# Optimization experiments

Measured on AMD Instinct MI355X. Metric: run time of the kernel, lower is better.

The kernel has to match this reference:

```python
import jax, jax.numpy as jnp
import numpy as np
from jax import lax

B, N, C = 8, 2000, 81            # batch, proposals, classes
MAX_INST = 100                    # config.detection_max_instances
MIN_CONF = 0.05                   # config.detection_min_confidence
NMS_THR = 0.3                     # config.detection_nms_threshold
H, W = 512, 512                   # config.image_shape[:2]
CLASS_OFFSET = 2.0                # > window extent, separates classes for batched NMS


def setup_inputs() -> dict:
    key = jax.random.key(0)
    k1, k2, k3, k4 = jax.random.split(key, 4)
    # valid normalized boxes (y1<y2, x1<x2)
    ctr = jax.random.uniform(k1, (B, N, 2))
    sz = jax.random.uniform(k2, (B, N, 2), minval=0.02, maxval=0.25)
    lo = jnp.clip(ctr - sz / 2, 0.0, 1.0)
    hi = jnp.clip(ctr + sz / 2, 0.0, 1.0)
    rois = jnp.stack([lo[..., 0], lo[..., 1], hi[..., 0], hi[..., 1]], axis=-1)
    probs = jax.nn.softmax(4.0 * jax.random.normal(k3, (B, N, C)), axis=-1)
    deltas = 0.1 * jax.random.normal(k4, (B, N, C, 4))
    bbox_std_dev = jnp.array([0.1, 0.1, 0.2, 0.2], jnp.float32)
    return {"rois": rois, "probs": probs, "deltas": deltas,
            "bbox_std_dev": bbox_std_dev}


def _apply_box_deltas(boxes, d):
    # boxes [N,4] (y1,x1,y2,x2), d [N,4] (dy,dx,log dh,log dw)
    h = boxes[:, 2] - boxes[:, 0]
    w = boxes[:, 3] - boxes[:, 1]
    cy = boxes[:, 0] + 0.5 * h + d[:, 0] * h
    cx = boxes[:, 1] + 0.5 * w + d[:, 1] * w
    h = h * jnp.exp(d[:, 2])
    w = w * jnp.exp(d[:, 3])
    return jnp.stack([cy - 0.5 * h, cx - 0.5 * w, cy + 0.5 * h, cx + 0.5 * w], axis=1)


def _pairwise_iou(b):
    # b [N,4] -> [N,N]
    area = (b[:, 2] - b[:, 0]) * (b[:, 3] - b[:, 1])
    yy1 = jnp.maximum(b[:, None, 0], b[None, :, 0])
    xx1 = jnp.maximum(b[:, None, 1], b[None, :, 1])
    yy2 = jnp.minimum(b[:, None, 2], b[None, :, 2])
    xx2 = jnp.minimum(b[:, None, 3], b[None, :, 3])
    inter = jnp.maximum(yy2 - yy1, 0.0) * jnp.maximum(xx2 - xx1, 0.0)
    union = area[:, None] + area[None, :] - inter
    return inter / jnp.maximum(union, 1e-12)


def _refine_one(rois, probs, deltas, bbox_std_dev):
    # rois [N,4], probs [N,C], deltas [N,C,4]
    cls = jnp.argmax(probs, axis=1)                       # [N] int
    idx = jnp.arange(N)
    scores = probs[idx, cls]                              # [N]
    d = deltas[idx, cls] * bbox_std_dev                   # [N,4]
    refined = jnp.clip(_apply_box_deltas(rois, d), 0.0, 1.0)  # window (0,0,1,1)
    valid = (cls > 0) & (scores >= MIN_CONF)
    # sort by score desc; invalid last
    order = jnp.argsort(-jnp.where(valid, scores, -jnp.inf))
    b = refined[order]
    s = scores[order]
    c = cls[order]
    v = valid[order]
    # per-class NMS via class-offset trick (equivalent to per-class NMS)
    ob = b + CLASS_OFFSET * c[:, None].astype(b.dtype)
    iou = _pairwise_iou(ob)                               # [N,N]

    def body(i, carry):
        keep, counts = carry
        sup = jnp.any(keep & (iou[i] > NMS_THR))
        ci = c[i]
        ok = v[i] & (~sup) & (counts[ci] < MAX_INST)      # per-class max_output_size
        return keep.at[i].set(ok), counts.at[ci].add(ok.astype(jnp.int32))

    keep, _ = lax.fori_loop(0, N, body,
                            (jnp.zeros((N,), bool), jnp.zeros((C,), jnp.int32)))
    kscores = jnp.where(keep, s, -jnp.inf)
    topv, topi = lax.top_k(kscores, MAX_INST)             # global top-k, sorted
    dvalid = topv > -jnp.inf
    boxes = jnp.where(dvalid[:, None], b[topi], 0.0)
    cls_f = jnp.where(dvalid, c[topi].astype(jnp.float32), 0.0)
    scr = jnp.where(dvalid, topv, 0.0)
    return jnp.concatenate([boxes, cls_f[:, None], scr[:, None]], axis=1)  # [MAX_INST,6]


def _attention_mask(det):
    # det [B,MAX_INST,6]; padded rows are all-zero boxes -> cover no pixels
    ys = (jnp.arange(H, dtype=jnp.float32) + 0.5) / H
    xs = (jnp.arange(W, dtype=jnp.float32) + 0.5) / W
    iny = (ys >= det[:, :, 0:1]) & (ys < det[:, :, 2:3])  # [B,D,H]
    inx = (xs >= det[:, :, 1:2]) & (xs < det[:, :, 3:4])  # [B,D,W]
    m = jnp.einsum('bdh,bdw->bhw', iny.astype(jnp.float32), inx.astype(jnp.float32))
    return (m > 0).astype(jnp.float32)


def reference(rois, probs, deltas, bbox_std_dev):
    det = jax.vmap(lambda r, p, dl: _refine_one(r, p, dl, bbox_std_dev))(rois, probs, deltas)
    mask = _attention_mask(det)
    return det, mask
```

## Files before the change

kernel.cpp:

```cpp
#include <hip/hip_runtime.h>
#include <math.h>

#define BB 8
#define NN 2000
#define CC 81
#define NPAD 2048
#define MAXI 100
#define HH 512
#define WW 512

__global__ void k_refine(const float* __restrict__ rois,
                         const float* __restrict__ probs,
                         const float* __restrict__ deltas,
                         const float* __restrict__ stdv,
                         float* __restrict__ score, int* __restrict__ cls,
                         int* __restrict__ valid, float* __restrict__ box,
                         unsigned long long* __restrict__ gkeys) {
#pragma clang fp contract(off)
  int g = blockIdx.x * 4 + (threadIdx.x >> 6);
  if (g >= BB * NPAD) return;
  int lane = threadIdx.x & 63;
  int b = g >> 11, n = g & (NPAD - 1);
  if (n >= NN) {
    if (lane == 0) {
      unsigned u = __float_as_uint(-INFINITY);
      u = ~u;
      gkeys[b * NPAD + n] =
          ((unsigned long long)u << 32) | (0xFFFFFFFFu - (unsigned)n);
      valid[b * NPAD + n] = 0;
    }
    return;
  }
  const float* pp = probs + ((size_t)b * NN + n) * CC;
  float best = -INFINITY;
  int bc = CC;
  for (int c = lane; c < CC; c += 64) {
    float p = pp[c];
    if (p > best) { best = p; bc = c; }
  }
  for (int off = 32; off; off >>= 1) {
    float ob = __shfl_xor(best, off, 64);
    int oc = __shfl_xor(bc, off, 64);
    if (ob > best || (ob == best && oc < bc)) { best = ob; bc = oc; }
  }
  if (lane == 0) {
    int idx = b * NPAD + n;
    const float* r = rois + ((size_t)b * NN + n) * 4;
    const float* dd = deltas + (((size_t)b * NN + n) * CC + bc) * 4;
    float d0 = dd[0] * stdv[0], d1 = dd[1] * stdv[1];
    float d2 = dd[2] * stdv[2], d3 = dd[3] * stdv[3];
    float y1 = r[0], x1 = r[1], y2 = r[2], x2 = r[3];
    float h = y2 - y1, w = x2 - x1;
    float cy = y1 + 0.5f * h + d0 * h;
    float cx = x1 + 0.5f * w + d1 * w;
    h = h * (float)exp((double)d2);
    w = w * (float)exp((double)d3);
    float ny1 = cy - 0.5f * h, nx1 = cx - 0.5f * w;
    float ny2 = cy + 0.5f * h, nx2 = cx + 0.5f * w;
    ny1 = fminf(fmaxf(ny1, 0.f), 1.f);
    nx1 = fminf(fmaxf(nx1, 0.f), 1.f);
    ny2 = fminf(fmaxf(ny2, 0.f), 1.f);
    nx2 = fminf(fmaxf(nx2, 0.f), 1.f);
    box[idx * 4 + 0] = ny1;
    box[idx * 4 + 1] = nx1;
    box[idx * 4 + 2] = ny2;
    box[idx * 4 + 3] = nx2;
    score[idx] = best;
    cls[idx] = bc;
    int v = (bc > 0 && best >= 0.05f) ? 1 : 0;
    valid[idx] = v;
    float ks = v ? best : -INFINITY;
    unsigned u = __float_as_uint(ks);
    u = (u & 0x80000000u) ? ~u : (u | 0x80000000u);
    gkeys[idx] = ((unsigned long long)u << 32) | (0xFFFFFFFFu - (unsigned)n);
  }
}

__global__ void k_rankp(const unsigned long long* __restrict__ gkeys,
                        int* __restrict__ partial) {
  __shared__ unsigned long long sk[256];
  int blk = blockIdx.x;
  int jp = blk & 7, ip = (blk >> 3) & 7, b = blk >> 6;
  int tid = threadIdx.x;
  sk[tid] = gkeys[b * NPAD + jp * 256 + tid];
  unsigned long long myk = gkeys[b * NPAD + ip * 256 + tid];
  __syncthreads();
  int cnt = 0;
#pragma unroll 8
  for (int j = 0; j < 256; j++) cnt += (sk[j] > myk) ? 1 : 0;
  partial[(b * 8 + jp) * NPAD + ip * 256 + tid] = cnt;
}

__global__ void __launch_bounds__(256)
k_permnms(const int* __restrict__ partial, const float* __restrict__ score,
          const int* __restrict__ cls, const int* __restrict__ valid,
          const float* __restrict__ box, float* __restrict__ det) {
#pragma clang fp contract(off)
  __shared__ int sperm[NPAD];
  int b = blockIdx.x, tid = threadIdx.x;
  for (int e = tid; e < NPAD; e += 256) {
    int rank = 0;
#pragma unroll
    for (int jp = 0; jp < 8; jp++) rank += partial[(b * 8 + jp) * NPAD + e];
    sperm[rank] = e;
  }
  __syncthreads();
  if (tid >= 64) return;
  int lane = tid;
  int kept = 0;
  bool done = false;
  float k0y1 = 0.f, k0x1 = 0.f, k0y2 = 0.f, k0x2 = 0.f, k0a = 0.f;
  float k1y1 = 0.f, k1x1 = 0.f, k1y2 = 0.f, k1x2 = 0.f, k1a = 0.f;
  for (int base = 0; base < NN && !done; base += 64) {
    int pi = sperm[base + lane];
    int o = b * NPAD + pi;
    float4 bx = ((const float4*)box)[o];
    int lv = valid[o];
    int lc = cls[o];
    float lsc = score[o];
    int lim = (NN - base < 64) ? (NN - base) : 64;
    for (int j = 0; j < lim; j++) {
      int v = __shfl(lv, j, 64);
      if (!v) { done = true; break; }
      float y1 = __shfl(bx.x, j, 64);
      float x1 = __shfl(bx.y, j, 64);
      float y2 = __shfl(bx.z, j, 64);
      float x2 = __shfl(bx.w, j, 64);
      int c = __shfl(lc, j, 64);
      float off = 2.0f * (float)c;
      float oy1 = y1 + off, ox1 = x1 + off, oy2 = y2 + off, ox2 = x2 + off;
      float area_i = (oy2 - oy1) * (ox2 - ox1);
      bool pred = false;
      if (lane < kept) {
        float yy1 = fmaxf(oy1, k0y1), xx1 = fmaxf(ox1, k0x1);
        float yy2 = fminf(oy2, k0y2), xx2 = fminf(ox2, k0x2);
        float inter = fmaxf(yy2 - yy1, 0.f) * fmaxf(xx2 - xx1, 0.f);
        float uni = (area_i + k0a) - inter;
        pred = (inter / fmaxf(uni, 1e-12f)) > 0.3f;
      }
      if (64 + lane < kept) {
        float yy1 = fmaxf(oy1, k1y1), xx1 = fmaxf(ox1, k1x1);
        float yy2 = fminf(oy2, k1y2), xx2 = fminf(ox2, k1x2);
        float inter = fmaxf(yy2 - yy1, 0.f) * fmaxf(xx2 - xx1, 0.f);
        float uni = (area_i + k1a) - inter;
        pred = pred || ((inter / fmaxf(uni, 1e-12f)) > 0.3f);
      }
      if (__ballot(pred) == 0ULL) {
        if (kept < 64) {
          if (lane == kept) { k0y1 = oy1; k0x1 = ox1; k0y2 = oy2; k0x2 = ox2; k0a = area_i; }
        } else {
          if (lane == kept - 64) { k1y1 = oy1; k1x1 = ox1; k1y2 = oy2; k1x2 = ox2; k1a = area_i; }
        }
        float sc = __shfl(lsc, j, 64);
        if (lane == 0) {
          float* dr = det + ((size_t)b * MAXI + kept) * 6;
          dr[0] = y1; dr[1] = x1; dr[2] = y2; dr[3] = x2;
          dr[4] = (float)c; dr[5] = sc;
        }
        kept++;
        if (kept == MAXI) { done = true; break; }
      }
    }
  }
  int rem = (MAXI - kept) * 6;
  float* dr0 = det + ((size_t)b * MAXI + kept) * 6;
  for (int t = lane; t < rem; t += 64) dr0[t] = 0.f;
}

__global__ void k_mask(const float* __restrict__ det, float* __restrict__ mask) {
  __shared__ float lx1[MAXI], lx2[MAXI];
  __shared__ unsigned long long wmask[4];
  int x = blockIdx.x;
  int h = x & (HH - 1);
  int b = x >> 9;
  int tid = threadIdx.x;
  int wv = tid >> 6, ln = tid & 63;
  float ys = ((float)h + 0.5f) * (1.0f / 512.0f);
  bool inb = false;
  float bx1 = 0.f, bx2 = 0.f;
  if (tid < MAXI) {
    const float* dr = det + ((size_t)b * MAXI + tid) * 6;
    float y1 = dr[0], y2 = dr[2];
    bx1 = dr[1]; bx2 = dr[3];
    inb = (ys >= y1 && ys < y2);
  }
  unsigned long long bm = __ballot(inb);
  if (ln == 0) wmask[wv] = bm;
  __syncthreads();
  int n = __popcll(wmask[0]) + __popcll(wmask[1]);
  if (inb) {
    int pos = (wv ? __popcll(wmask[0]) : 0) +
              __popcll(bm & ((1ULL << ln) - 1ULL));
    lx1[pos] = bx1; lx2[pos] = bx2;
  }
  __syncthreads();
  float xs0 = ((float)tid + 0.5f) * (1.0f / 512.0f);
  float xs1 = ((float)(tid + 256) + 0.5f) * (1.0f / 512.0f);
  bool c0 = false, c1 = false;
  for (int t = 0; t < n; t++) {
    float a = lx1[t], bq = lx2[t];
    c0 = c0 || (xs0 >= a && xs0 < bq);
    c1 = c1 || (xs1 >= a && xs1 < bq);
  }
  float* row = mask + ((size_t)b * HH + h) * WW;
  row[tid] = c0 ? 1.0f : 0.0f;
  row[tid + 256] = c1 ? 1.0f : 0.0f;
}

extern "C" void kernel_launch(void* const* d_in, const int* in_sizes, int n_in,
                              void* d_out, int out_size, void* d_ws, size_t ws_size,
                              hipStream_t stream) {
  const float* rois = (const float*)d_in[0];
  const float* probs = (const float*)d_in[1];
  const float* deltas = (const float*)d_in[2];
  const float* stdv = (const float*)d_in[3];
  float* out = (float*)d_out;
  float* det = out;
  float* mask = out + BB * MAXI * 6;

  char* p = (char*)d_ws;
  unsigned long long* gkeys = (unsigned long long*)p; p += (size_t)BB * NPAD * 8;
  float* box     = (float*)p; p += (size_t)BB * NPAD * 16;
  float* score   = (float*)p; p += (size_t)BB * NPAD * 4;
  int*   cls     = (int*)p;   p += (size_t)BB * NPAD * 4;
  int*   valid   = (int*)p;   p += (size_t)BB * NPAD * 4;
  int*   partial = (int*)p;   p += (size_t)BB * 8 * NPAD * 4;

  k_refine<<<(BB * NPAD) / 4, 256, 0, stream>>>(rois, probs, deltas, stdv,
                                                score, cls, valid, box, gkeys);
  k_rankp<<<BB * 64, 256, 0, stream>>>(gkeys, partial);
  k_permnms<<<BB, 256, 0, stream>>>(partial, score, cls, valid, box, det);
  k_mask<<<BB * HH, 256, 0, stream>>>(det, mask);
}
```

Before: 136.3 us.

## Parallelize NMS with block-wide IoU bitmask tiles and a wave-level greedy scan

The single-wave sequential greedy NMS is replaced by a 256-wide tile scheme. All 256 threads first compute suppression against the already-kept boxes, then build a 256x256 pairwise IoU bitmask in shared memory. One wave then resolves the greedy keep order with ballots and bit operations, and writes the kept detections. This is meant to cut the long serial shuffle chain per candidate. In exchange it does a full 256x256 IoU tile of work per chunk and adds block-wide barriers.

```diff
diff --git a/kernel.cpp b/kernel.cpp
--- a/kernel.cpp
+++ b/kernel.cpp
@@ -97,74 +97,146 @@
           const float* __restrict__ box, float* __restrict__ det) {
 #pragma clang fp contract(off)
   __shared__ int sperm[NPAD];
+  __shared__ float4 spk4[256];
+  __shared__ float sarea[256];
+  __shared__ float4 sbox4[256];
+  __shared__ float sscr[256];
+  __shared__ int   scl[256];
+  __shared__ int   sval[256];
+  __shared__ int   sksup[256];
+  __shared__ unsigned long long smask[256][5];
+  __shared__ float4 kpk4[MAXI];
+  __shared__ float  karea[MAXI];
+  __shared__ int s_kcount, s_done;
+
   int b = blockIdx.x, tid = threadIdx.x;
+  int lane = tid & 63, wv = tid >> 6;
+
   for (int e = tid; e < NPAD; e += 256) {
     int rank = 0;
 #pragma unroll
     for (int jp = 0; jp < 8; jp++) rank += partial[(b * 8 + jp) * NPAD + e];
     sperm[rank] = e;
   }
+  if (tid == 0) { s_kcount = 0; s_done = 0; }
   __syncthreads();
-  if (tid >= 64) return;
-  int lane = tid;
-  int kept = 0;
-  bool done = false;
-  float k0y1 = 0.f, k0x1 = 0.f, k0y2 = 0.f, k0x2 = 0.f, k0a = 0.f;
-  float k1y1 = 0.f, k1x1 = 0.f, k1y2 = 0.f, k1x2 = 0.f, k1a = 0.f;
-  for (int base = 0; base < NN && !done; base += 64) {
-    int pi = sperm[base + lane];
-    int o = b * NPAD + pi;
-    float4 bx = ((const float4*)box)[o];
-    int lv = valid[o];
-    int lc = cls[o];
-    float lsc = score[o];
-    int lim = (NN - base < 64) ? (NN - base) : 64;
-    for (int j = 0; j < lim; j++) {
-      int v = __shfl(lv, j, 64);
-      if (!v) { done = true; break; }
-      float y1 = __shfl(bx.x, j, 64);
-      float x1 = __shfl(bx.y, j, 64);
-      float y2 = __shfl(bx.z, j, 64);
-      float x2 = __shfl(bx.w, j, 64);
-      int c = __shfl(lc, j, 64);
+
+  int prevkept = 0;
+  for (int base = 0;; base += 256) {
+    {
+      int i = base + tid;
+      float4 bx = make_float4(0.f, 0.f, 0.f, 0.f);
+      int c = 0, v = 0;
+      float sc = 0.f;
+      if (i < NN) {
+        int o = b * NPAD + sperm[i];
+        bx = ((const float4*)box)[o];
+        c = cls[o]; v = valid[o]; sc = score[o];
+      }
       float off = 2.0f * (float)c;
-      float oy1 = y1 + off, ox1 = x1 + off, oy2 = y2 + off, ox2 = x2 + off;
-      float area_i = (oy2 - oy1) * (ox2 - ox1);
-      bool pred = false;
-      if (lane < kept) {
-        float yy1 = fmaxf(oy1, k0y1), xx1 = fmaxf(ox1, k0x1);
-        float yy2 = fminf(oy2, k0y2), xx2 = fminf(ox2, k0x2);
+      float oy1 = bx.x + off, ox1 = bx.y + off;
+      float oy2 = bx.z + off, ox2 = bx.w + off;
+      float ar = (oy2 - oy1) * (ox2 - ox1);
+      if (!v) { oy1 = ox1 = oy2 = ox2 = 0.f; ar = 0.f; }
+      spk4[tid] = make_float4(oy1, ox1, oy2, ox2);
+      sarea[tid] = ar;
+      sbox4[tid] = bx;
+      sscr[tid] = sc; scl[tid] = c; sval[tid] = v;
+    }
+    __syncthreads();
+    {
+      float4 me = spk4[tid];
+      float ma = sarea[tid];
+      int ks = 0;
+      int kc = s_kcount;
+      for (int t = 0; t < kc; t++) {
+        float4 kb = kpk4[t];
+        float yy1 = fmaxf(me.x, kb.x), xx1 = fmaxf(me.y, kb.y);
+        float yy2 = fminf(me.z, kb.z), xx2 = fminf(me.w, kb.w);
         float inter = fmaxf(yy2 - yy1, 0.f) * fmaxf(xx2 - xx1, 0.f);
-        float uni = (area_i + k0a) - inter;
-        pred = (inter / fmaxf(uni, 1e-12f)) > 0.3f;
-      }
-      if (64 + lane < kept) {
-        float yy1 = fmaxf(oy1, k1y1), xx1 = fmaxf(ox1, k1x1);
-        float yy2 = fminf(oy2, k1y2), xx2 = fminf(ox2, k1x2);
+        float uni = (ma + karea[t]) - inter;
+        if (inter / fmaxf(uni, 1e-12f) > 0.3f) ks = 1;
+      }
+      sksup[tid] = ks;
+      unsigned long long m0 = 0, m1 = 0, m2 = 0, m3 = 0;
+      for (int j = 0; j < 256; j++) {
+        float4 ob = spk4[j];
+        float yy1 = fmaxf(me.x, ob.x), xx1 = fmaxf(me.y, ob.y);
+        float yy2 = fminf(me.z, ob.z), xx2 = fminf(me.w, ob.w);
         float inter = fmaxf(yy2 - yy1, 0.f) * fmaxf(xx2 - xx1, 0.f);
-        float uni = (area_i + k1a) - inter;
-        pred = pred || ((inter / fmaxf(uni, 1e-12f)) > 0.3f);
-      }
-      if (__ballot(pred) == 0ULL) {
-        if (kept < 64) {
-          if (lane == kept) { k0y1 = oy1; k0x1 = ox1; k0y2 = oy2; k0x2 = ox2; k0a = area_i; }
-        } else {
-          if (lane == kept - 64) { k1y1 = oy1; k1x1 = ox1; k1y2 = oy2; k1x2 = ox2; k1a = area_i; }
+        float uni = (ma + sarea[j]) - inter;
+        unsigned long long bit =
+            (inter / fmaxf(uni, 1e-12f) > 0.3f) ? 1ULL : 0ULL;
+        if (j < 64) m0 |= bit << j;
+        else if (j < 128) m1 |= bit << (j - 64);
+        else if (j < 192) m2 |= bit << (j - 128);
+        else m3 |= bit << (j - 192);
+      }
+      smask[tid][0] = m0; smask[tid][1] = m1;
+      smask[tid][2] = m2; smask[tid][3] = m3;
+    }
+    __syncthreads();
+    if (wv == 0) {
+      unsigned long long m[4][4];
+      int rv[4], ok4[4];
+      for (int s = 0; s < 4; s++) {
+        int i = s * 64 + lane;
+        m[s][0] = smask[i][0]; m[s][1] = smask[i][1];
+        m[s][2] = smask[i][2]; m[s][3] = smask[i][3];
+        rv[s] = sval[i];
+        ok4[s] = rv[s] && !sksup[i];
+      }
+      unsigned long long vb0 = __ballot(rv[0] != 0);
+      unsigned long long vb1 = __ballot(rv[1] != 0);
+      unsigned long long vb2 = __ballot(rv[2] != 0);
+      unsigned long long vb3 = __ballot(rv[3] != 0);
+      bool all_valid = (vb0 & vb1 & vb2 & vb3) == ~0ULL;
+      unsigned long long acc[4] = {0ULL, 0ULL, 0ULL, 0ULL};
+      int kcount = prevkept;
+      bool stop = false;
+      for (int s = 0; s < 4 && !stop; s++) {
+        bool ok = ok4[s] && (((m[s][0] & acc[0]) | (m[s][1] & acc[1]) |
+                              (m[s][2] & acc[2]) | (m[s][3] & acc[3])) == 0ULL);
+        unsigned long long bal = __ballot(ok);
+        while (bal) {
+          int o = __ffsll((unsigned long long)bal) - 1;
+          acc[s] |= 1ULL << o;
+          kcount++;
+          if (kcount == MAXI) { stop = true; break; }
+          bool conf = ((m[s][s] >> o) & 1ULL) != 0ULL;
+          ok = ok && !conf && (lane != o);
+          bal = __ballot(ok);
         }
-        float sc = __shfl(lsc, j, 64);
-        if (lane == 0) {
-          float* dr = det + ((size_t)b * MAXI + kept) * 6;
-          dr[0] = y1; dr[1] = x1; dr[2] = y2; dr[3] = x2;
-          dr[4] = (float)c; dr[5] = sc;
+      }
+      int prefix[4], run = 0;
+      for (int s = 0; s < 4; s++) { prefix[s] = run; run += (int)__popcll(acc[s]); }
+      for (int s = 0; s < 4; s++) {
+        if ((acc[s] >> lane) & 1ULL) {
+          int i = s * 64 + lane;
+          int row = prevkept + prefix[s] +
+                    (int)__popcll(acc[s] & ((1ULL << lane) - 1ULL));
+          float4 bx = sbox4[i];
+          float* dr = det + ((size_t)b * MAXI + row) * 6;
+          dr[0] = bx.x; dr[1] = bx.y; dr[2] = bx.z; dr[3] = bx.w;
+          dr[4] = (float)scl[i]; dr[5] = sscr[i];
+          kpk4[row] = spk4[i];
+          karea[row] = sarea[i];
         }
-        kept++;
-        if (kept == MAXI) { done = true; break; }
+      }
+      if (lane == 0) {
+        s_kcount = kcount;
+        s_done = (kcount >= MAXI) || !all_valid || (base + 256 >= NN) ? 1 : 0;
       }
     }
-  }
-  int rem = (MAXI - kept) * 6;
-  float* dr0 = det + ((size_t)b * MAXI + kept) * 6;
-  for (int t = lane; t < rem; t += 64) dr0[t] = 0.f;
+    __syncthreads();
+    prevkept = s_kcount;
+    if (s_done) break;
+  }
+  {
+    int rem = (MAXI - prevkept) * 6;
+    float* dr0 = det + ((size_t)b * MAXI + prevkept) * 6;
+    for (int t = tid; t < rem; t += 256) dr0[t] = 0.f;
+  }
 }
 
 __global__ void k_mask(const float* __restrict__ det, float* __restrict__ mask) {
```

New measurement: 163.3 us. 1.2x slower.

## Precompute IoU bitmask for top-256 candidates and resolve NMS via ballots

Applied to the files above, without the earlier changes.

Grows the NMS block to 1024 threads. The block builds a 256x256 pairwise suppression bitmask in shared memory for the top-ranked candidates, then one wave resolves greedy NMS with bitmask ANDs and ballot loops instead of one serial IoU pass per candidate. The old serial shuffle loop is kept as a fallback for candidates past 256, and only runs when fewer than MAXI boxes are kept and all 256 were valid. This targets the long serial dependency chain in single-wave NMS, in exchange for more shared memory and an extra O(256^2) IoU computation.

```diff
diff --git a/kernel.cpp b/kernel.cpp
--- a/kernel.cpp
+++ b/kernel.cpp
@@ -91,80 +91,193 @@
   partial[(b * 8 + jp) * NPAD + ip * 256 + tid] = cnt;
 }
 
-__global__ void __launch_bounds__(256)
+__global__ void __launch_bounds__(1024)
 k_permnms(const int* __restrict__ partial, const float* __restrict__ score,
           const int* __restrict__ cls, const int* __restrict__ valid,
           const float* __restrict__ box, float* __restrict__ det) {
 #pragma clang fp contract(off)
   __shared__ int sperm[NPAD];
+  __shared__ float4 spk4[256];
+  __shared__ float sarea[256];
+  __shared__ float4 sbox4[256];
+  __shared__ float sscr[256];
+  __shared__ int   scl[256];
+  __shared__ int   sval[256];
+  __shared__ unsigned long long smask[256][5];
+  __shared__ float4 kpk4[MAXI];
+  __shared__ float  karea[MAXI];
+  __shared__ int s_kcount, s_need;
+
   int b = blockIdx.x, tid = threadIdx.x;
-  for (int e = tid; e < NPAD; e += 256) {
+  int lane = tid & 63, wv = tid >> 6;
+
+  for (int e = tid; e < NPAD; e += 1024) {
     int rank = 0;
 #pragma unroll
     for (int jp = 0; jp < 8; jp++) rank += partial[(b * 8 + jp) * NPAD + e];
     sperm[rank] = e;
   }
-  __syncthreads();
-  if (tid >= 64) return;
-  int lane = tid;
-  int kept = 0;
-  bool done = false;
-  float k0y1 = 0.f, k0x1 = 0.f, k0y2 = 0.f, k0x2 = 0.f, k0a = 0.f;
-  float k1y1 = 0.f, k1x1 = 0.f, k1y2 = 0.f, k1x2 = 0.f, k1a = 0.f;
-  for (int base = 0; base < NN && !done; base += 64) {
-    int pi = sperm[base + lane];
-    int o = b * NPAD + pi;
+  if (tid == 0) { s_kcount = 0; s_need = 0; }
+  __syncthreads();
+
+  if (tid < 256) {
+    int o = b * NPAD + sperm[tid];
     float4 bx = ((const float4*)box)[o];
-    int lv = valid[o];
-    int lc = cls[o];
-    float lsc = score[o];
-    int lim = (NN - base < 64) ? (NN - base) : 64;
-    for (int j = 0; j < lim; j++) {
-      int v = __shfl(lv, j, 64);
-      if (!v) { done = true; break; }
-      float y1 = __shfl(bx.x, j, 64);
-      float x1 = __shfl(bx.y, j, 64);
-      float y2 = __shfl(bx.z, j, 64);
-      float x2 = __shfl(bx.w, j, 64);
-      int c = __shfl(lc, j, 64);
-      float off = 2.0f * (float)c;
-      float oy1 = y1 + off, ox1 = x1 + off, oy2 = y2 + off, ox2 = x2 + off;
-      float area_i = (oy2 - oy1) * (ox2 - ox1);
-      bool pred = false;
-      if (lane < kept) {
-        float yy1 = fmaxf(oy1, k0y1), xx1 = fmaxf(ox1, k0x1);
-        float yy2 = fminf(oy2, k0y2), xx2 = fminf(ox2, k0x2);
-        float inter = fmaxf(yy2 - yy1, 0.f) * fmaxf(xx2 - xx1, 0.f);
-        float uni = (area_i + k0a) - inter;
-        pred = (inter / fmaxf(uni, 1e-12f)) > 0.3f;
+    int c = cls[o], v = valid[o];
+    float sc = score[o];
+    float off = 2.0f * (float)c;
+    float oy1 = bx.x + off, ox1 = bx.y + off;
+    float oy2 = bx.z + off, ox2 = bx.w + off;
+    float ar = (oy2 - oy1) * (ox2 - ox1);
+    if (!v) { oy1 = ox1 = oy2 = ox2 = 0.f; ar = 0.f; }
+    spk4[tid] = make_float4(oy1, ox1, oy2, ox2);
+    sarea[tid] = ar;
+    sbox4[tid] = bx;
+    sscr[tid] = sc; scl[tid] = c; sval[tid] = v;
+  }
+  __syncthreads();
+
+  {
+    int i = tid & 255, jw = tid >> 8;
+    float4 me = spk4[i];
+    float ma = sarea[i];
+    int j0 = jw * 64;
+    unsigned long long m = 0ULL;
+#pragma unroll 8
+    for (int jj = 0; jj < 64; jj++) {
+      float4 ob = spk4[j0 + jj];
+      float yy1 = fmaxf(me.x, ob.x), xx1 = fmaxf(me.y, ob.y);
+      float yy2 = fminf(me.z, ob.z), xx2 = fminf(me.w, ob.w);
+      float inter = fmaxf(yy2 - yy1, 0.f) * fmaxf(xx2 - xx1, 0.f);
+      float uni = (ma + sarea[j0 + jj]) - inter;
+      if (inter / fmaxf(uni, 1e-12f) > 0.3f) m |= 1ULL << jj;
+    }
+    smask[i][jw] = m;
+  }
+  __syncthreads();
+
+  if (wv == 0) {
+    unsigned long long m[4][4];
+    int vv[4];
+    for (int s = 0; s < 4; s++) {
+      int i = s * 64 + lane;
+      m[s][0] = smask[i][0]; m[s][1] = smask[i][1];
+      m[s][2] = smask[i][2]; m[s][3] = smask[i][3];
+      vv[s] = sval[i];
+    }
+    bool all_valid = ((__ballot(vv[0] != 0) & __ballot(vv[1] != 0) &
+                       __ballot(vv[2] != 0) & __ballot(vv[3] != 0)) == ~0ULL);
+    unsigned long long acc[4] = {0ULL, 0ULL, 0ULL, 0ULL};
+    int kcount = 0;
+    bool stop = false;
+    for (int s = 0; s < 4 && !stop; s++) {
+      bool ok = vv[s] && (((m[s][0] & acc[0]) | (m[s][1] & acc[1]) |
+                           (m[s][2] & acc[2]) | (m[s][3] & acc[3])) == 0ULL);
+      unsigned long long bal = __ballot(ok);
+      while (bal) {
+        int o = __ffsll((unsigned long long)bal) - 1;
+        acc[s] |= 1ULL << o;
+        kcount++;
+        if (kcount == MAXI) { stop = true; break; }
+        ok = ok && !((m[s][s] >> o) & 1ULL) && (lane != o);
+        bal = __ballot(ok);
       }
-      if (64 + lane < kept) {
-        float yy1 = fmaxf(oy1, k1y1), xx1 = fmaxf(ox1, k1x1);
-        float yy2 = fminf(oy2, k1y2), xx2 = fminf(ox2, k1x2);
-        float inter = fmaxf(yy2 - yy1, 0.f) * fmaxf(xx2 - xx1, 0.f);
-        float uni = (area_i + k1a) - inter;
-        pred = pred || ((inter / fmaxf(uni, 1e-12f)) > 0.3f);
+    }
+    int prefix[4], run = 0;
+    for (int s = 0; s < 4; s++) { prefix[s] = run; run += (int)__popcll(acc[s]); }
+    for (int s = 0; s < 4; s++) {
+      if ((acc[s] >> lane) & 1ULL) {
+        int i = s * 64 + lane;
+        int row = prefix[s] + (int)__popcll(acc[s] & ((1ULL << lane) - 1ULL));
+        float4 bx = sbox4[i];
+        float* dr = det + ((size_t)b * MAXI + row) * 6;
+        dr[0] = bx.x; dr[1] = bx.y; dr[2] = bx.z; dr[3] = bx.w;
+        dr[4] = (float)scl[i]; dr[5] = sscr[i];
+        kpk4[row] = spk4[i];
+        karea[row] = sarea[i];
       }
-      if (__ballot(pred) == 0ULL) {
-        if (kept < 64) {
-          if (lane == kept) { k0y1 = oy1; k0x1 = ox1; k0y2 = oy2; k0x2 = ox2; k0a = area_i; }
-        } else {
-          if (lane == kept - 64) { k1y1 = oy1; k1x1 = ox1; k1y2 = oy2; k1x2 = ox2; k1a = area_i; }
+    }
+    if (lane == 0) {
+      s_kcount = kcount;
+      s_need = (kcount < MAXI && all_valid) ? 1 : 0;
+    }
+  }
+  __syncthreads();
+
+  if (s_need && wv == 0) {
+    int kept = s_kcount;
+    float k0y1 = 0.f, k0x1 = 0.f, k0y2 = 0.f, k0x2 = 0.f, k0a = 0.f;
+    float k1y1 = 0.f, k1x1 = 0.f, k1y2 = 0.f, k1x2 = 0.f, k1a = 0.f;
+    if (lane < kept) {
+      float4 t = kpk4[lane];
+      k0y1 = t.x; k0x1 = t.y; k0y2 = t.z; k0x2 = t.w; k0a = karea[lane];
+    }
+    if (64 + lane < kept) {
+      float4 t = kpk4[64 + lane];
+      k1y1 = t.x; k1x1 = t.y; k1y2 = t.z; k1x2 = t.w; k1a = karea[64 + lane];
+    }
+    bool done = false;
+    for (int base = 256; base < NN && !done; base += 64) {
+      int pi = sperm[base + lane];
+      int o = b * NPAD + pi;
+      float4 bx = ((const float4*)box)[o];
+      int lv = valid[o];
+      int lc = cls[o];
+      float lsc = score[o];
+      int lim = (NN - base < 64) ? (NN - base) : 64;
+      for (int j = 0; j < lim; j++) {
+        int v = __shfl(lv, j, 64);
+        if (!v) { done = true; break; }
+        float y1 = __shfl(bx.x, j, 64);
+        float x1 = __shfl(bx.y, j, 64);
+        float y2 = __shfl(bx.z, j, 64);
+        float x2 = __shfl(bx.w, j, 64);
+        int c = __shfl(lc, j, 64);
+        float off = 2.0f * (float)c;
+        float oy1 = y1 + off, ox1 = x1 + off, oy2 = y2 + off, ox2 = x2 + off;
+        float area_i = (oy2 - oy1) * (ox2 - ox1);
+        bool pred = false;
+        if (lane < kept) {
+          float yy1 = fmaxf(oy1, k0y1), xx1 = fmaxf(ox1, k0x1);
+          float yy2 = fminf(oy2, k0y2), xx2 = fminf(ox2, k0x2);
+          float inter = fmaxf(yy2 - yy1, 0.f) * fmaxf(xx2 - xx1, 0.f);
+          float uni = (area_i + k0a) - inter;
+          pred = (inter / fmaxf(uni, 1e-12f)) > 0.3f;
         }
-        float sc = __shfl(lsc, j, 64);
-        if (lane == 0) {
-          float* dr = det + ((size_t)b * MAXI + kept) * 6;
-          dr[0] = y1; dr[1] = x1; dr[2] = y2; dr[3] = x2;
-          dr[4] = (float)c; dr[5] = sc;
+        if (64 + lane < kept) {
+          float yy1 = fmaxf(oy1, k1y1), xx1 = fmaxf(ox1, k1x1);
+          float yy2 = fminf(oy2, k1y2), xx2 = fminf(ox2, k1x2);
+          float inter = fmaxf(yy2 - yy1, 0.f) * fmaxf(xx2 - xx1, 0.f);
+          float uni = (area_i + k1a) - inter;
+          pred = pred || ((inter / fmaxf(uni, 1e-12f)) > 0.3f);
         }
-        kept++;
-        if (kept == MAXI) { done = true; break; }
+        if (__ballot(pred) == 0ULL) {
+          if (kept < 64) {
+            if (lane == kept) { k0y1 = oy1; k0x1 = ox1; k0y2 = oy2; k0x2 = ox2; k0a = area_i; }
+          } else {
+            if (lane == kept - 64) { k1y1 = oy1; k1x1 = ox1; k1y2 = oy2; k1x2 = ox2; k1a = area_i; }
+          }
+          float sc = __shfl(lsc, j, 64);
+          if (lane == 0) {
+            float* dr = det + ((size_t)b * MAXI + kept) * 6;
+            dr[0] = y1; dr[1] = x1; dr[2] = y2; dr[3] = x2;
+            dr[4] = (float)c; dr[5] = sc;
+          }
+          kept++;
+          if (kept == MAXI) { done = true; break; }
+        }
       }
     }
-  }
-  int rem = (MAXI - kept) * 6;
-  float* dr0 = det + ((size_t)b * MAXI + kept) * 6;
-  for (int t = lane; t < rem; t += 64) dr0[t] = 0.f;
+    if (lane == 0) s_kcount = kept;
+  }
+  __syncthreads();
+
+  {
+    int kc = s_kcount;
+    int rem = (MAXI - kc) * 6;
+    float* dr0 = det + ((size_t)b * MAXI + kc) * 6;
+    for (int t = tid; t < rem; t += 1024) dr0[t] = 0.f;
+  }
 }
 
 __global__ void k_mask(const float* __restrict__ det, float* __restrict__ mask) {
@@ -229,6 +342,6 @@
   k_refine<<<(BB * NPAD) / 4, 256, 0, stream>>>(rois, probs, deltas, stdv,
                                                 score, cls, valid, box, gkeys);
   k_rankp<<<BB * 64, 256, 0, stream>>>(gkeys, partial);
-  k_permnms<<<BB, 256, 0, stream>>>(partial, score, cls, valid, box, det);
+  k_permnms<<<BB, 1024, 0, stream>>>(partial, score, cls, valid, box, det);
   k_mask<<<BB * HH, 256, 0, stream>>>(det, mask);
 }
```

Result: faster. 123.5 us (-9.4%).
